# Kernel optimization log

Measured on AMD Instinct MI355X. Metric: run time of the kernel, lower is better.

Reference implementation:

```python
import jax, jax.numpy as jnp
import numpy as np

N_NODES = 100_000
N_EDGES = 6_400_000
CH = 5


def setup_inputs() -> dict:
    key = jax.random.key(0)
    ks = jax.random.split(key, 16)
    inp = {
        "x": jax.random.normal(ks[0], (N_NODES, 2), dtype=jnp.float32),
        "edge_index": jax.random.randint(ks[1], (2, N_EDGES), 0, N_NODES, dtype=jnp.int64 if jax.config.jax_enable_x64 else jnp.int32).astype(jnp.int32),
        "edge_attr": jax.random.uniform(ks[2], (N_EDGES, 1), dtype=jnp.float32),
        "lin1_w": jax.random.normal(ks[3], (2, CH), dtype=jnp.float32) * 0.5,
        "lin1_b": jax.random.normal(ks[4], (CH,), dtype=jnp.float32) * 0.1,
        "conv1_wf": jax.random.normal(ks[5], (2 * CH + 1, CH), dtype=jnp.float32) * 0.3,
        "conv1_bf": jax.random.normal(ks[6], (CH,), dtype=jnp.float32) * 0.1,
        "conv1_ws": jax.random.normal(ks[7], (2 * CH + 1, CH), dtype=jnp.float32) * 0.3,
        "conv1_bs": jax.random.normal(ks[8], (CH,), dtype=jnp.float32) * 0.1,
        "conv2_wf": jax.random.normal(ks[9], (2 * CH + 1, CH), dtype=jnp.float32) * 0.3,
        "conv2_bf": jax.random.normal(ks[10], (CH,), dtype=jnp.float32) * 0.1,
        "conv2_ws": jax.random.normal(ks[11], (2 * CH + 1, CH), dtype=jnp.float32) * 0.3,
        "conv2_bs": jax.random.normal(ks[12], (CH,), dtype=jnp.float32) * 0.1,
        "lin2_w": jax.random.normal(ks[13], (CH, 2), dtype=jnp.float32) * 0.5,
        "lin2_b": jax.random.normal(ks[14], (2,), dtype=jnp.float32) * 0.1,
    }
    return inp


def cgconv(x, edge_index, edge_attr, wf, bf, ws, bs):
    # PyG CGConv: x_i' = x_i + sum_{j->i} sigmoid(z W_f + b_f) * softplus(z W_s + b_s)
    # z = [x_i, x_j, e_ij]; edge_index[0]=source j, edge_index[1]=target i
    src, dst = edge_index[0], edge_index[1]
    z = jnp.concatenate([x[dst], x[src], edge_attr], axis=-1)  # [E, 2C+dim]
    msg = jax.nn.sigmoid(z @ wf + bf) * jax.nn.softplus(z @ ws + bs)  # [E, C]
    agg = jax.ops.segment_sum(msg, dst, num_segments=x.shape[0])  # [N, C]
    return x + agg


def reference(x, edge_index, edge_attr,
              lin1_w, lin1_b,
              conv1_wf, conv1_bf, conv1_ws, conv1_bs,
              conv2_wf, conv2_bf, conv2_ws, conv2_bs,
              lin2_w, lin2_b):
    h = x @ lin1_w + lin1_b  # [N, C]
    h = cgconv(h, edge_index, edge_attr, conv1_wf, conv1_bf, conv1_ws, conv1_bs)
    h = cgconv(h, edge_index, edge_attr, conv2_wf, conv2_bf, conv2_ws, conv2_bs)
    return h @ lin2_w + lin2_b  # [N, 2]
```

## Files before the change

### kernel.cpp

```cpp
#include <hip/hip_runtime.h>
#include <hip/hip_fp16.h>

constexpr int NN = 100000;
constexpr int NE = 6400000;
constexpr int BSH = 7;
constexpr int BN = 1 << BSH;
constexpr int NBUCK = (NN + BN - 1) / BN;
constexpr int BCAP = 9216;
constexpr int STILE = 8192;
constexpr int NSB = (NE + STILE - 1) / STILE;
constexpr int NP = 1024;

#define LOG2E 1.44269504f
#define LN2   0.69314718f


__device__ __forceinline__ void prep_core(const float hv[5],
                                          const float* __restrict__ wf,
                                          const float* __restrict__ bf,
                                          const float* __restrict__ ws,
                                          const float* __restrict__ bs,
                                          int n, float* __restrict__ TD,
                                          unsigned short* __restrict__ TSh) {
    float tg[5], ts[5], sg[5], ss[5];
#pragma unroll
    for (int c = 0; c < 5; ++c) {
        float a = bf[c], d = bs[c], u = 0.f, v = 0.f;
#pragma unroll
        for (int k = 0; k < 5; ++k) {
            a += hv[k] * wf[k * 5 + c];
            d += hv[k] * ws[k * 5 + c];
            u += hv[k] * wf[(5 + k) * 5 + c];
            v += hv[k] * ws[(5 + k) * 5 + c];
        }
        tg[c] = -a * LOG2E; ts[c] = -d * LOG2E;
        sg[c] = -u * LOG2E; ss[c] = -v * LOG2E;
    }
    float4* Dp = (float4*)(TD + (size_t)n * 12);
    Dp[0] = make_float4(tg[0], tg[1], tg[2], tg[3]);
    Dp[1] = make_float4(tg[4], ts[0], ts[1], ts[2]);
    Dp[2] = make_float4(ts[3], ts[4], 0.f, 0.f);

    unsigned p[5];
#pragma unroll
    for (int c = 0; c < 5; ++c) {
        unsigned lo = (unsigned)__half_as_ushort(__float2half_rn(sg[c]));
        unsigned hi = (unsigned)__half_as_ushort(__float2half_rn(ss[c]));
        p[c] = lo | (hi << 16);
    }
    uint4 w0 = make_uint4(p[0], p[1], p[2], p[3]);
    uint4 w1 = make_uint4(p[4], 0u, 0u, 0u);
    *(uint4*)(TSh + (size_t)n * 16) = w0;
    *(uint4*)(TSh + (size_t)n * 16 + 8) = w1;
}

__global__ __launch_bounds__(256) void k_prep1(const float* __restrict__ x,
                                               const float* __restrict__ l1w,
                                               const float* __restrict__ l1b,
                                               const float* __restrict__ wf,
                                               const float* __restrict__ bf,
                                               const float* __restrict__ ws,
                                               const float* __restrict__ bs,
                                               float* __restrict__ TD,
                                               unsigned short* __restrict__ TSh,
                                               float* __restrict__ h) {
    int n = blockIdx.x * 256 + threadIdx.x;
    if (n >= NN) return;
    float x0 = x[2 * n], x1 = x[2 * n + 1];
    float hv[5];
#pragma unroll
    for (int c = 0; c < 5; ++c) {
        hv[c] = l1b[c] + x0 * l1w[c] + x1 * l1w[5 + c];
        h[(size_t)n * 5 + c] = hv[c];
    }
    prep_core(hv, wf, bf, ws, bs, n, TD, TSh);
}

__global__ __launch_bounds__(256) void k_initcurs(int* __restrict__ gcurs) {
    int i = blockIdx.x * 256 + threadIdx.x;
    if (i < NBUCK) gcurs[i] = i * BCAP;
}

__global__ __launch_bounds__(512) void k_scatter4(const int* __restrict__ ei,
                                                  const float* __restrict__ ea,
                                                  int* __restrict__ gcurs,
                                                  unsigned int* __restrict__ rec) {
    __shared__ unsigned int lrec[STILE];
    __shared__ unsigned int spk[STILE];
    __shared__ int C[NBUCK];
    __shared__ int loc[NBUCK];
    __shared__ int gbase[NBUCK];
    __shared__ int A[NP];
    __shared__ int wsum[16];
    const int tid = threadIdx.x, blk = blockIdx.x;
    const int base = blk * STILE;
    const int m = min(STILE, NE - base);

    for (int i = tid; i < NBUCK; i += 512) C[i] = 0;
    __syncthreads();

    const int m4 = m >> 2;
    const int4* s4 = (const int4*)(ei + base);
    const int4* d4 = (const int4*)(ei + NE + base);
    const float4* a4 = (const float4*)(ea + base);
    for (int q = tid; q < m4; q += 512) {
        int4 s = s4[q];
        int4 d = d4[q];
        float4 a = a4[q];
        int k = q * 4;
        lrec[k + 0] = (unsigned)s.x | ((unsigned)(d.x & (BN - 1)) << 17) |
                      (__float2uint_rn(a.x * 255.f) << 24);
        lrec[k + 1] = (unsigned)s.y | ((unsigned)(d.y & (BN - 1)) << 17) |
                      (__float2uint_rn(a.y * 255.f) << 24);
        lrec[k + 2] = (unsigned)s.z | ((unsigned)(d.z & (BN - 1)) << 17) |
                      (__float2uint_rn(a.z * 255.f) << 24);
        lrec[k + 3] = (unsigned)s.w | ((unsigned)(d.w & (BN - 1)) << 17) |
                      (__float2uint_rn(a.w * 255.f) << 24);
        atomicAdd(&C[(unsigned)d.x >> BSH], 1);
        atomicAdd(&C[(unsigned)d.y >> BSH], 1);
        atomicAdd(&C[(unsigned)d.z >> BSH], 1);
        atomicAdd(&C[(unsigned)d.w >> BSH], 1);
    }
    __syncthreads();

    for (int b = tid; b < NBUCK; b += 512)
        gbase[b] = C[b] ? atomicAdd(&gcurs[b], C[b]) : 0;

    const int lane = tid & 63;
    const int wv = tid >> 6;
    int orig[2], incl[2];
#pragma unroll
    for (int half = 0; half < 2; ++half) {
        int c = wv + half * 8;
        int i = c * 64 + lane;
        int v = (i < NBUCK) ? C[i] : 0;
        orig[half] = v;
#pragma unroll
        for (int off = 1; off < 64; off <<= 1) {
            int t = __shfl_up(v, off, 64);
            if (lane >= off) v += t;
        }
        incl[half] = v;
        if (lane == 63) wsum[c] = v;
    }
    __syncthreads();
    if (tid < 16) {
        int v = wsum[tid];
#pragma unroll
        for (int off = 1; off < 16; off <<= 1) {
            int t = __shfl_up(v, off, 16);
            if (tid >= off) v += t;
        }
        wsum[tid] = v;
    }
    __syncthreads();
#pragma unroll
    for (int half = 0; half < 2; ++half) {
        int c = wv + half * 8;
        int i = c * 64 + lane;
        int coff = (c > 0) ? wsum[c - 1] : 0;
        int excl = incl[half] - orig[half] + coff;
        A[i] = excl;
        if (i < NBUCK) loc[i] = excl;
    }
    __syncthreads();

    for (int k = tid; k < m; k += 512) {
        int bkt = (unsigned)ei[NE + base + k] >> BSH;
        int p = atomicAdd(&loc[bkt], 1);
        spk[p] = (unsigned)k | ((unsigned)bkt << 16);
    }
    __syncthreads();

    for (int p = tid; p < m; p += 512) {
        unsigned pk = spk[p];
        int k = pk & 0xFFFF;
        int bkt = pk >> 16;
        rec[gbase[bkt] + (p - A[bkt])] = lrec[k];
    }
}

__global__ __launch_bounds__(512) void k_sortbkt(const int* __restrict__ gcurs,
                                                 unsigned int* __restrict__ rec,
                                                 int2* __restrict__ nrange) {
    __shared__ unsigned int lrec[BCAP];
    __shared__ int cnt[BN];
    __shared__ int curs[BN];
    const int b = blockIdx.x, tid = threadIdx.x;
    const int e0 = b * BCAP;
    const int m = gcurs[b] - e0;
    const int node0 = b << BSH;
    const int nloc = min(BN, NN - node0);

    for (int i = tid; i < m; i += 512) lrec[i] = rec[e0 + i];
    if (tid < BN) cnt[tid] = 0;
    __syncthreads();
    for (int i = tid; i < m; i += 512)
        atomicAdd(&cnt[(lrec[i] >> 17) & (BN - 1)], 1);
    __syncthreads();

    if (tid < 64) {
        int v0 = cnt[tid];
        int i0 = v0;
#pragma unroll
        for (int off = 1; off < 64; off <<= 1) {
            int t = __shfl_up(i0, off, 64);
            if (tid >= off) i0 += t;
        }
        int tot0 = __shfl(i0, 63, 64);
        int v1 = cnt[64 + tid];
        int i1 = v1;
#pragma unroll
        for (int off = 1; off < 64; off <<= 1) {
            int t = __shfl_up(i1, off, 64);
            if (tid >= off) i1 += t;
        }
        i1 += tot0;
        int e0x = i0 - v0;
        int e1x = i1 - v1;
        curs[tid] = e0x;
        curs[64 + tid] = e1x;
        if (tid < nloc)
            nrange[node0 + tid] = make_int2(e0 + e0x, e0 + e0x + v0);
        if (64 + tid < nloc)
            nrange[node0 + 64 + tid] = make_int2(e0 + e1x, e0 + e1x + v1);
    }
    __syncthreads();
    for (int i = tid; i < m; i += 512) {
        unsigned int r = lrec[i];
        int dl = (r >> 17) & (BN - 1);
        int pos = atomicAdd(&curs[dl], 1);
        rec[e0 + pos] = r;
    }
}

__device__ __forceinline__ void conv_core(
        const unsigned int* __restrict__ rec, const int2 rg,
        const float4* __restrict__ Dp, const unsigned short* __restrict__ TSh,
        const __half2 we2[5], float acc[5]) {
    const int lane = threadIdx.x & 15;
    float4 d0 = Dp[0], d1 = Dp[1], d2 = Dp[2];
    __half2 dd2[5];
    dd2[0] = __floats2half2_rn(d0.x, d1.y);
    dd2[1] = __floats2half2_rn(d0.y, d1.z);
    dd2[2] = __floats2half2_rn(d0.z, d1.w);
    dd2[3] = __floats2half2_rn(d0.w, d2.x);
    dd2[4] = __floats2half2_rn(d1.x, d2.y);
    const __half2 one2 = __float2half2_rn(1.f);
    const __half hz = __float2half(0.f);

#pragma unroll
    for (int c = 0; c < 5; ++c) acc[c] = 0.f;
    const int eEnd = rg.y;
    for (int e = rg.x + lane; e < eEnd; e += 64) {
        unsigned r[4];
        bool vld[4];
        float4 q0[4];
        unsigned q1[4];
        __half2 a2[4];
#pragma unroll
        for (int j = 0; j < 4; ++j) {
            int ej = e + j * 16;
            vld[j] = ej < eEnd;
            r[j] = rec[vld[j] ? ej : e];
        }
#pragma unroll
        for (int j = 0; j < 4; ++j) {
            const unsigned src = r[j] & 0x1FFFFu;
            const unsigned short* row = TSh + (size_t)src * 16;
            q0[j] = *(const float4*)row;
            q1[j] = *(const unsigned*)(row + 8);
            a2[j] = __float2half2_rn((float)(r[j] >> 24) * (1.f / 255.f));
        }
#pragma unroll
        for (int j = 0; j < 4; ++j) {
            if (!vld[j]) continue;
            union { float4 f; __half2 h2[4]; } u; u.f = q0[j];
            __half2 s2[5] = {u.h2[0], u.h2[1], u.h2[2], u.h2[3],
                             *(__half2*)&q1[j]};
#pragma unroll
            for (int c = 0; c < 5; ++c) {
                __half2 z2 = __hadd2(__hfma2(a2[j], we2[c], dd2[c]), s2[c]);
                __half zx = __low2half(z2);
                __half zy = __high2half(z2);
                __half nab = __hmin(zy, __hneg(zy));
                __half2 e2 = h2exp2(__halves2half2(zx, nab));
                __half2 o2 = __hadd2(e2, one2);
                float sig = __half2float(hrcp(__low2half(o2)));
                float lg  = __half2float(hlog2(__high2half(o2)));
                float mx  = __half2float(__hmin(zy, hz));
                acc[c] = fmaf(sig, lg - mx, acc[c]);
            }
        }
    }
#pragma unroll
    for (int off = 8; off >= 1; off >>= 1)
#pragma unroll
        for (int c = 0; c < 5; ++c)
            acc[c] += __shfl_xor(acc[c], off, 16);
}

__global__ __launch_bounds__(256) void k_conv_prep(
        const unsigned int* __restrict__ rec, const int2* __restrict__ nrange,
        const float* __restrict__ TD, const unsigned short* __restrict__ TSh,
        const float* __restrict__ wf, const float* __restrict__ ws,
        const float* __restrict__ wf2, const float* __restrict__ bf2,
        const float* __restrict__ ws2, const float* __restrict__ bs2,
        float* __restrict__ h,
        float* __restrict__ TD2, unsigned short* __restrict__ TSh2) {
    const int tid = threadIdx.x;
    const int lane = tid & 15;
    const int n = blockIdx.x * 16 + (tid >> 4);

    __half2 we2[5];
#pragma unroll
    for (int c = 0; c < 5; ++c)
        we2[c] = __floats2half2_rn(-wf[50 + c] * LOG2E, -ws[50 + c] * LOG2E);

    float acc[5];
    conv_core(rec, nrange[n], (const float4*)(TD + (size_t)n * 12), TSh,
              we2, acc);

    float hv[5];
#pragma unroll
    for (int c = 0; c < 5; ++c)
        hv[c] = h[(size_t)n * 5 + c] + LN2 * acc[c];
    if (lane == 0) {
#pragma unroll
        for (int c = 0; c < 5; ++c) h[(size_t)n * 5 + c] = hv[c];
    }
    if (lane < 5) {
        const int c = lane;
        float a = bf2[c], d = bs2[c], u = 0.f, v = 0.f;
#pragma unroll
        for (int k = 0; k < 5; ++k) {
            a += hv[k] * wf2[k * 5 + c];
            d += hv[k] * ws2[k * 5 + c];
            u += hv[k] * wf2[(5 + k) * 5 + c];
            v += hv[k] * ws2[(5 + k) * 5 + c];
        }
        TD2[(size_t)n * 12 + c]     = -a * LOG2E;
        TD2[(size_t)n * 12 + 5 + c] = -d * LOG2E;
        unsigned lo = (unsigned)__half_as_ushort(__float2half_rn(-u * LOG2E));
        unsigned hi = (unsigned)__half_as_ushort(__float2half_rn(-v * LOG2E));
        ((unsigned*)(TSh2 + (size_t)n * 16))[c] = lo | (hi << 16);
    }
}

__global__ __launch_bounds__(256) void k_conv_out(
        const unsigned int* __restrict__ rec, const int2* __restrict__ nrange,
        const float* __restrict__ TD, const unsigned short* __restrict__ TSh,
        const float* __restrict__ wf, const float* __restrict__ ws,
        const float* __restrict__ h,
        const float* __restrict__ l2w, const float* __restrict__ l2b,
        float* __restrict__ out) {
    const int tid = threadIdx.x;
    const int lane = tid & 15;
    const int n = blockIdx.x * 16 + (tid >> 4);

    __half2 we2[5];
#pragma unroll
    for (int c = 0; c < 5; ++c)
        we2[c] = __floats2half2_rn(-wf[50 + c] * LOG2E, -ws[50 + c] * LOG2E);

    float acc[5];
    conv_core(rec, nrange[n], (const float4*)(TD + (size_t)n * 12), TSh,
              we2, acc);

    if (lane == 0) {
        float o0 = l2b[0], o1 = l2b[1];
#pragma unroll
        for (int c = 0; c < 5; ++c) {
            float hv = h[(size_t)n * 5 + c] + LN2 * acc[c];
            o0 += hv * l2w[2 * c];
            o1 += hv * l2w[2 * c + 1];
        }
        out[2 * n] = o0;
        out[2 * n + 1] = o1;
    }
}

__global__ __launch_bounds__(256) void k_prep_fb(const float* __restrict__ h,
                                                 const float* __restrict__ wf,
                                                 const float* __restrict__ bf,
                                                 const float* __restrict__ ws,
                                                 const float* __restrict__ bs,
                                                 float* __restrict__ T,
                                                 float* __restrict__ S,
                                                 float* __restrict__ hout) {
    int n = blockIdx.x * 256 + threadIdx.x;
    if (n >= NN) return;
    float hv[5];
#pragma unroll
    for (int k = 0; k < 5; ++k) hv[k] = h[5 * n + k];
    float tf[5], ts[5], sf[5], ss[5];
#pragma unroll
    for (int c = 0; c < 5; ++c) {
        float a = bf[c], d = bs[c], u = 0.f, v = 0.f;
#pragma unroll
        for (int k = 0; k < 5; ++k) {
            a += hv[k] * wf[k * 5 + c];
            d += hv[k] * ws[k * 5 + c];
            u += hv[k] * wf[(5 + k) * 5 + c];
            v += hv[k] * ws[(5 + k) * 5 + c];
        }
        tf[c] = a; ts[c] = d; sf[c] = u; ss[c] = v;
    }
    float4* Tp = (float4*)(T + (size_t)n * 16);
    Tp[0] = make_float4(tf[0], tf[1], tf[2], tf[3]);
    Tp[1] = make_float4(tf[4], ts[0], ts[1], ts[2]);
    Tp[2] = make_float4(ts[3], ts[4], 0.f, 0.f);
    float4* Sp = (float4*)(S + (size_t)n * 16);
    Sp[0] = make_float4(sf[0], sf[1], sf[2], sf[3]);
    Sp[1] = make_float4(sf[4], ss[0], ss[1], ss[2]);
    Sp[2] = make_float4(ss[3], ss[4], 0.f, 0.f);
#pragma unroll
    for (int c = 0; c < 5; ++c) hout[5 * n + c] = hv[c];
}

__global__ __launch_bounds__(256) void k_conv_atomic(const int* __restrict__ ei,
                                                     const float* __restrict__ ea,
                                                     const float* __restrict__ T,
                                                     const float* __restrict__ S,
                                                     const float* __restrict__ wf,
                                                     const float* __restrict__ ws,
                                                     float* __restrict__ hout) {
    int e = blockIdx.x * 256 + threadIdx.x;
    if (e >= NE) return;
    int src = ei[e];
    int dst = ei[NE + e];
    float a = ea[e];
    const float4* Tp = (const float4*)(T + (size_t)dst * 16);
    const float4* Sp = (const float4*)(S + (size_t)src * 16);
    float4 t0 = Tp[0], t1 = Tp[1], t2 = Tp[2];
    float4 s0 = Sp[0], s1 = Sp[1], s2 = Sp[2];
    float za[5] = {t0.x + s0.x, t0.y + s0.y, t0.z + s0.z, t0.w + s0.w, t1.x + s1.x};
    float zs[5] = {t1.y + s1.y, t1.z + s1.z, t1.w + s1.w, t2.x + s2.x, t2.y + s2.y};
    float* outp = hout + (size_t)dst * 5;
#pragma unroll
    for (int c = 0; c < 5; ++c) {
        float f = za[c] + a * wf[50 + c];
        float s = zs[c] + a * ws[50 + c];
        float sig = 1.f / (1.f + __expf(-f));
        float sp = __logf(1.f + __expf(-fabsf(s))) + fmaxf(s, 0.f);
        unsafeAtomicAdd(outp + c, sig * sp);
    }
}

__global__ __launch_bounds__(256) void k_lin1_fb(const float* __restrict__ x,
                                                 const float* __restrict__ w,
                                                 const float* __restrict__ b,
                                                 float* __restrict__ h) {
    int n = blockIdx.x * 256 + threadIdx.x;
    if (n >= NN) return;
    float x0 = x[2 * n], x1 = x[2 * n + 1];
#pragma unroll
    for (int c = 0; c < 5; ++c)
        h[5 * n + c] = b[c] + x0 * w[c] + x1 * w[5 + c];
}

__global__ __launch_bounds__(256) void k_lin2_fb(const float* __restrict__ h,
                                                 const float* __restrict__ w,
                                                 const float* __restrict__ b,
                                                 float* __restrict__ out) {
    int n = blockIdx.x * 256 + threadIdx.x;
    if (n >= NN) return;
    float o0 = b[0], o1 = b[1];
#pragma unroll
    for (int c = 0; c < 5; ++c) {
        float hv = h[(size_t)n * 5 + c];
        o0 += hv * w[2 * c];
        o1 += hv * w[2 * c + 1];
    }
    out[2 * n] = o0;
    out[2 * n + 1] = o1;
}

extern "C" void kernel_launch(void* const* d_in, const int* in_sizes, int n_in,
                              void* d_out, int out_size, void* d_ws, size_t ws_size,
                              hipStream_t stream) {
    const float* x    = (const float*)d_in[0];
    const int*   ei   = (const int*)d_in[1];
    const float* ea   = (const float*)d_in[2];
    const float* l1w  = (const float*)d_in[3];
    const float* l1b  = (const float*)d_in[4];
    const float* c1wf = (const float*)d_in[5];
    const float* c1bf = (const float*)d_in[6];
    const float* c1ws = (const float*)d_in[7];
    const float* c1bs = (const float*)d_in[8];
    const float* c2wf = (const float*)d_in[9];
    const float* c2bf = (const float*)d_in[10];
    const float* c2ws = (const float*)d_in[11];
    const float* c2bs = (const float*)d_in[12];
    const float* l2w  = (const float*)d_in[13];
    const float* l2b  = (const float*)d_in[14];
    float* out = (float*)d_out;
    char* ws = (char*)d_ws;

    size_t o_rec    = 0;
    size_t o_nrange = o_rec + (size_t)NBUCK * BCAP * 4;
    size_t o_gcurs  = o_nrange + (size_t)NN * 8;
    size_t o_TD1    = (o_gcurs + (size_t)NBUCK * 4 + 15) & ~(size_t)15;
    size_t o_TS1    = o_TD1 + (size_t)NN * 12 * 4;
    size_t o_TD2    = o_TS1 + (size_t)NN * 16 * 2;
    size_t o_TS2    = o_TD2 + (size_t)NN * 12 * 4;
    size_t o_h      = o_TS2 + (size_t)NN * 16 * 2;
    size_t need     = o_h + (size_t)NN * 5 * 4;

    int nb_n = (NN + 255) / 256;

    if (ws_size >= need) {
        unsigned int* rec    = (unsigned int*)(ws + o_rec);
        int2* nrange         = (int2*)(ws + o_nrange);
        int* gcurs           = (int*)(ws + o_gcurs);
        float* TD1           = (float*)(ws + o_TD1);
        unsigned short* TS1  = (unsigned short*)(ws + o_TS1);
        float* TD2           = (float*)(ws + o_TD2);
        unsigned short* TS2  = (unsigned short*)(ws + o_TS2);
        float* h             = (float*)(ws + o_h);

        k_initcurs<<<(NBUCK + 255) / 256, 256, 0, stream>>>(gcurs);
        k_scatter4<<<NSB,   512, 0, stream>>>(ei, ea, gcurs, rec);
        k_sortbkt <<<NBUCK, 512, 0, stream>>>(gcurs, rec, nrange);

        k_prep1<<<nb_n, 256, 0, stream>>>(x, l1w, l1b,
                                          c1wf, c1bf, c1ws, c1bs, TD1, TS1, h);
        k_conv_prep<<<NN / 16, 256, 0, stream>>>(rec, nrange, TD1, TS1,
                                                 c1wf, c1ws,
                                                 c2wf, c2bf, c2ws, c2bs,
                                                 h, TD2, TS2);
        k_conv_out<<<NN / 16, 256, 0, stream>>>(rec, nrange, TD2, TS2,
                                                c2wf, c2ws, h, l2w, l2b, out);
    } else {
        float* h0 = (float*)(ws);
        float* h1 = (float*)(ws + 2000000);
        float* h2 = h0;
        float* T  = (float*)(ws + 4000000);
        float* S  = (float*)(ws + 10400000);
        int nb_e = (NE + 255) / 256;

        k_lin1_fb<<<nb_n, 256, 0, stream>>>(x, l1w, l1b, h0);
        k_prep_fb<<<nb_n, 256, 0, stream>>>(h0, c1wf, c1bf, c1ws, c1bs, T, S, h1);
        k_conv_atomic<<<nb_e, 256, 0, stream>>>(ei, ea, T, S, c1wf, c1ws, h1);
        k_prep_fb<<<nb_n, 256, 0, stream>>>(h1, c2wf, c2bf, c2ws, c2bs, T, S, h2);
        k_conv_atomic<<<nb_e, 256, 0, stream>>>(ei, ea, T, S, c2wf, c2ws, h2);
        k_lin2_fb<<<nb_n, 256, 0, stream>>>(h2, l2w, l2b, out);
    }
}
```

Baseline: 187.9 us.

## Drop per-node sort; aggregate each bucket's edges with shared-memory atomics

Removes the k_sortbkt pass that sorted each destination bucket by node and built per-node ranges. The conv kernels now run one 512-thread block per 128-node bucket, stream its unsorted edges, and accumulate messages into a shared-memory array with atomic adds, keeping destination terms in shared memory. This saves a full read/write pass over the edge records and the nrange array. The cost is heavy contention on shared-memory float atomics (about 64 edges per node, 5 channels), plus nondeterministic summation order and fewer, larger blocks (782).

```diff
diff --git a/kernel.cpp b/kernel.cpp
--- a/kernel.cpp
+++ b/kernel.cpp
@@ -180,198 +180,112 @@
     }
 }
 
-__global__ __launch_bounds__(512) void k_sortbkt(const int* __restrict__ gcurs,
-                                                 unsigned int* __restrict__ rec,
-                                                 int2* __restrict__ nrange) {
-    __shared__ unsigned int lrec[BCAP];
-    __shared__ int cnt[BN];
-    __shared__ int curs[BN];
-    const int b = blockIdx.x, tid = threadIdx.x;
-    const int e0 = b * BCAP;
-    const int m = gcurs[b] - e0;
-    const int node0 = b << BSH;
-    const int nloc = min(BN, NN - node0);
-
-    for (int i = tid; i < m; i += 512) lrec[i] = rec[e0 + i];
-    if (tid < BN) cnt[tid] = 0;
-    __syncthreads();
-    for (int i = tid; i < m; i += 512)
-        atomicAdd(&cnt[(lrec[i] >> 17) & (BN - 1)], 1);
-    __syncthreads();
-
-    if (tid < 64) {
-        int v0 = cnt[tid];
-        int i0 = v0;
-#pragma unroll
-        for (int off = 1; off < 64; off <<= 1) {
-            int t = __shfl_up(i0, off, 64);
-            if (tid >= off) i0 += t;
-        }
-        int tot0 = __shfl(i0, 63, 64);
-        int v1 = cnt[64 + tid];
-        int i1 = v1;
-#pragma unroll
-        for (int off = 1; off < 64; off <<= 1) {
-            int t = __shfl_up(i1, off, 64);
-            if (tid >= off) i1 += t;
-        }
-        i1 += tot0;
-        int e0x = i0 - v0;
-        int e1x = i1 - v1;
-        curs[tid] = e0x;
-        curs[64 + tid] = e1x;
-        if (tid < nloc)
-            nrange[node0 + tid] = make_int2(e0 + e0x, e0 + e0x + v0);
-        if (64 + tid < nloc)
-            nrange[node0 + 64 + tid] = make_int2(e0 + e1x, e0 + e1x + v1);
-    }
-    __syncthreads();
-    for (int i = tid; i < m; i += 512) {
-        unsigned int r = lrec[i];
-        int dl = (r >> 17) & (BN - 1);
-        int pos = atomicAdd(&curs[dl], 1);
-        rec[e0 + pos] = r;
-    }
-}
-
-__device__ __forceinline__ void conv_core(
-        const unsigned int* __restrict__ rec, const int2 rg,
-        const float4* __restrict__ Dp, const unsigned short* __restrict__ TSh,
-        const __half2 we2[5], float acc[5]) {
-    const int lane = threadIdx.x & 15;
-    float4 d0 = Dp[0], d1 = Dp[1], d2 = Dp[2];
-    __half2 dd2[5];
-    dd2[0] = __floats2half2_rn(d0.x, d1.y);
-    dd2[1] = __floats2half2_rn(d0.y, d1.z);
-    dd2[2] = __floats2half2_rn(d0.z, d1.w);
-    dd2[3] = __floats2half2_rn(d0.w, d2.x);
-    dd2[4] = __floats2half2_rn(d1.x, d2.y);
+__device__ __forceinline__ void bucket_conv_core(
+        const unsigned int* __restrict__ rec, int e0, int m,
+        const unsigned short* __restrict__ TSh,
+        const float* __restrict__ TD, int node0, int nloc,
+        const float* __restrict__ wf, const float* __restrict__ ws,
+        float* accf , __half2* sdd2 ) {
+    const int tid = threadIdx.x;
+    __half2 we2[5];
+#pragma unroll
+    for (int c = 0; c < 5; ++c)
+        we2[c] = __floats2half2_rn(-wf[50 + c] * LOG2E, -ws[50 + c] * LOG2E);
+
+    if (tid < nloc) {
+        const float4* Dp = (const float4*)(TD + (size_t)(node0 + tid) * 12);
+        float4 d0 = Dp[0], d1 = Dp[1], d2 = Dp[2];
+        sdd2[tid * 5 + 0] = __floats2half2_rn(d0.x, d1.y);
+        sdd2[tid * 5 + 1] = __floats2half2_rn(d0.y, d1.z);
+        sdd2[tid * 5 + 2] = __floats2half2_rn(d0.z, d1.w);
+        sdd2[tid * 5 + 3] = __floats2half2_rn(d0.w, d2.x);
+        sdd2[tid * 5 + 4] = __floats2half2_rn(d1.x, d2.y);
+    }
+    for (int i = tid; i < BN * 5; i += 512) accf[i] = 0.f;
+    __syncthreads();
+
     const __half2 one2 = __float2half2_rn(1.f);
     const __half hz = __float2half(0.f);
-
-#pragma unroll
-    for (int c = 0; c < 5; ++c) acc[c] = 0.f;
-    const int eEnd = rg.y;
-    for (int e = rg.x + lane; e < eEnd; e += 64) {
-        unsigned r[4];
-        bool vld[4];
-        float4 q0[4];
-        unsigned q1[4];
-        __half2 a2[4];
-#pragma unroll
-        for (int j = 0; j < 4; ++j) {
-            int ej = e + j * 16;
-            vld[j] = ej < eEnd;
-            r[j] = rec[vld[j] ? ej : e];
-        }
-#pragma unroll
-        for (int j = 0; j < 4; ++j) {
-            const unsigned src = r[j] & 0x1FFFFu;
-            const unsigned short* row = TSh + (size_t)src * 16;
-            q0[j] = *(const float4*)row;
-            q1[j] = *(const unsigned*)(row + 8);
-            a2[j] = __float2half2_rn((float)(r[j] >> 24) * (1.f / 255.f));
-        }
-#pragma unroll
-        for (int j = 0; j < 4; ++j) {
-            if (!vld[j]) continue;
-            union { float4 f; __half2 h2[4]; } u; u.f = q0[j];
-            __half2 s2[5] = {u.h2[0], u.h2[1], u.h2[2], u.h2[3],
-                             *(__half2*)&q1[j]};
-#pragma unroll
-            for (int c = 0; c < 5; ++c) {
-                __half2 z2 = __hadd2(__hfma2(a2[j], we2[c], dd2[c]), s2[c]);
-                __half zx = __low2half(z2);
-                __half zy = __high2half(z2);
-                __half nab = __hmin(zy, __hneg(zy));
-                __half2 e2 = h2exp2(__halves2half2(zx, nab));
-                __half2 o2 = __hadd2(e2, one2);
-                float sig = __half2float(hrcp(__low2half(o2)));
-                float lg  = __half2float(hlog2(__high2half(o2)));
-                float mx  = __half2float(__hmin(zy, hz));
-                acc[c] = fmaf(sig, lg - mx, acc[c]);
-            }
-        }
-    }
-#pragma unroll
-    for (int off = 8; off >= 1; off >>= 1)
-#pragma unroll
-        for (int c = 0; c < 5; ++c)
-            acc[c] += __shfl_xor(acc[c], off, 16);
-}
-
-__global__ __launch_bounds__(256) void k_conv_prep(
-        const unsigned int* __restrict__ rec, const int2* __restrict__ nrange,
+    for (int i = tid; i < m; i += 512) {
+        const unsigned r = rec[e0 + i];
+        const unsigned src = r & 0x1FFFFu;
+        const int dl = (r >> 17) & (BN - 1);
+        const unsigned short* row = TSh + (size_t)src * 16;
+        float4 q0 = *(const float4*)row;
+        unsigned q1 = *(const unsigned*)(row + 8);
+        __half2 a2 = __float2half2_rn((float)(r >> 24) * (1.f / 255.f));
+        union { float4 f; __half2 h2[4]; } u; u.f = q0;
+        __half2 s2[5] = {u.h2[0], u.h2[1], u.h2[2], u.h2[3], *(__half2*)&q1};
+#pragma unroll
+        for (int c = 0; c < 5; ++c) {
+            __half2 z2 = __hadd2(__hfma2(a2, we2[c], sdd2[dl * 5 + c]), s2[c]);
+            __half zx = __low2half(z2);
+            __half zy = __high2half(z2);
+            __half nab = __hmin(zy, __hneg(zy));
+            __half2 e2 = h2exp2(__halves2half2(zx, nab));
+            __half2 o2 = __hadd2(e2, one2);
+            float sig = __half2float(hrcp(__low2half(o2)));
+            float lg  = __half2float(hlog2(__high2half(o2)));
+            float mx  = __half2float(__hmin(zy, hz));
+            unsafeAtomicAdd(&accf[dl * 5 + c], sig * (lg - mx));
+        }
+    }
+    __syncthreads();
+}
+
+__global__ __launch_bounds__(512) void k_conv_prep(
+        const unsigned int* __restrict__ rec, const int* __restrict__ gcurs,
         const float* __restrict__ TD, const unsigned short* __restrict__ TSh,
         const float* __restrict__ wf, const float* __restrict__ ws,
         const float* __restrict__ wf2, const float* __restrict__ bf2,
         const float* __restrict__ ws2, const float* __restrict__ bs2,
         float* __restrict__ h,
         float* __restrict__ TD2, unsigned short* __restrict__ TSh2) {
-    const int tid = threadIdx.x;
-    const int lane = tid & 15;
-    const int n = blockIdx.x * 16 + (tid >> 4);
-
-    __half2 we2[5];
-#pragma unroll
-    for (int c = 0; c < 5; ++c)
-        we2[c] = __floats2half2_rn(-wf[50 + c] * LOG2E, -ws[50 + c] * LOG2E);
-
-    float acc[5];
-    conv_core(rec, nrange[n], (const float4*)(TD + (size_t)n * 12), TSh,
-              we2, acc);
-
-    float hv[5];
-#pragma unroll
-    for (int c = 0; c < 5; ++c)
-        hv[c] = h[(size_t)n * 5 + c] + LN2 * acc[c];
-    if (lane == 0) {
-#pragma unroll
-        for (int c = 0; c < 5; ++c) h[(size_t)n * 5 + c] = hv[c];
-    }
-    if (lane < 5) {
-        const int c = lane;
-        float a = bf2[c], d = bs2[c], u = 0.f, v = 0.f;
-#pragma unroll
-        for (int k = 0; k < 5; ++k) {
-            a += hv[k] * wf2[k * 5 + c];
-            d += hv[k] * ws2[k * 5 + c];
-            u += hv[k] * wf2[(5 + k) * 5 + c];
-            v += hv[k] * ws2[(5 + k) * 5 + c];
-        }
-        TD2[(size_t)n * 12 + c]     = -a * LOG2E;
-        TD2[(size_t)n * 12 + 5 + c] = -d * LOG2E;
-        unsigned lo = (unsigned)__half_as_ushort(__float2half_rn(-u * LOG2E));
-        unsigned hi = (unsigned)__half_as_ushort(__float2half_rn(-v * LOG2E));
-        ((unsigned*)(TSh2 + (size_t)n * 16))[c] = lo | (hi << 16);
-    }
-}
-
-__global__ __launch_bounds__(256) void k_conv_out(
-        const unsigned int* __restrict__ rec, const int2* __restrict__ nrange,
+    __shared__ float accf[BN * 5];
+    __shared__ __half2 sdd2[BN * 5];
+    const int b = blockIdx.x, tid = threadIdx.x;
+    const int e0 = b * BCAP;
+    const int m = gcurs[b] - e0;
+    const int node0 = b << BSH;
+    const int nloc = min(BN, NN - node0);
+
+    bucket_conv_core(rec, e0, m, TSh, TD, node0, nloc, wf, ws, accf, sdd2);
+
+    if (tid < nloc) {
+        const int n = node0 + tid;
+        float hv[5];
+#pragma unroll
+        for (int c = 0; c < 5; ++c) {
+            hv[c] = h[(size_t)n * 5 + c] + LN2 * accf[tid * 5 + c];
+            h[(size_t)n * 5 + c] = hv[c];
+        }
+        prep_core(hv, wf2, bf2, ws2, bs2, n, TD2, TSh2);
+    }
+}
+
+__global__ __launch_bounds__(512) void k_conv_out(
+        const unsigned int* __restrict__ rec, const int* __restrict__ gcurs,
         const float* __restrict__ TD, const unsigned short* __restrict__ TSh,
         const float* __restrict__ wf, const float* __restrict__ ws,
         const float* __restrict__ h,
         const float* __restrict__ l2w, const float* __restrict__ l2b,
         float* __restrict__ out) {
-    const int tid = threadIdx.x;
-    const int lane = tid & 15;
-    const int n = blockIdx.x * 16 + (tid >> 4);
-
-    __half2 we2[5];
-#pragma unroll
-    for (int c = 0; c < 5; ++c)
-        we2[c] = __floats2half2_rn(-wf[50 + c] * LOG2E, -ws[50 + c] * LOG2E);
-
-    float acc[5];
-    conv_core(rec, nrange[n], (const float4*)(TD + (size_t)n * 12), TSh,
-              we2, acc);
-
-    if (lane == 0) {
+    __shared__ float accf[BN * 5];
+    __shared__ __half2 sdd2[BN * 5];
+    const int b = blockIdx.x, tid = threadIdx.x;
+    const int e0 = b * BCAP;
+    const int m = gcurs[b] - e0;
+    const int node0 = b << BSH;
+    const int nloc = min(BN, NN - node0);
+
+    bucket_conv_core(rec, e0, m, TSh, TD, node0, nloc, wf, ws, accf, sdd2);
+
+    if (tid < nloc) {
+        const int n = node0 + tid;
         float o0 = l2b[0], o1 = l2b[1];
 #pragma unroll
         for (int c = 0; c < 5; ++c) {
-            float hv = h[(size_t)n * 5 + c] + LN2 * acc[c];
+            float hv = h[(size_t)n * 5 + c] + LN2 * accf[tid * 5 + c];
             o0 += hv * l2w[2 * c];
             o1 += hv * l2w[2 * c + 1];
         }
@@ -498,8 +412,7 @@
     char* ws = (char*)d_ws;
 
     size_t o_rec    = 0;
-    size_t o_nrange = o_rec + (size_t)NBUCK * BCAP * 4;
-    size_t o_gcurs  = o_nrange + (size_t)NN * 8;
+    size_t o_gcurs  = o_rec + (size_t)NBUCK * BCAP * 4;
     size_t o_TD1    = (o_gcurs + (size_t)NBUCK * 4 + 15) & ~(size_t)15;
     size_t o_TS1    = o_TD1 + (size_t)NN * 12 * 4;
     size_t o_TD2    = o_TS1 + (size_t)NN * 16 * 2;
@@ -511,7 +424,6 @@
 
     if (ws_size >= need) {
         unsigned int* rec    = (unsigned int*)(ws + o_rec);
-        int2* nrange         = (int2*)(ws + o_nrange);
         int* gcurs           = (int*)(ws + o_gcurs);
         float* TD1           = (float*)(ws + o_TD1);
         unsigned short* TS1  = (unsigned short*)(ws + o_TS1);
@@ -520,17 +432,16 @@
         float* h             = (float*)(ws + o_h);
 
         k_initcurs<<<(NBUCK + 255) / 256, 256, 0, stream>>>(gcurs);
-        k_scatter4<<<NSB,   512, 0, stream>>>(ei, ea, gcurs, rec);
-        k_sortbkt <<<NBUCK, 512, 0, stream>>>(gcurs, rec, nrange);
+        k_scatter4<<<NSB, 512, 0, stream>>>(ei, ea, gcurs, rec);
 
         k_prep1<<<nb_n, 256, 0, stream>>>(x, l1w, l1b,
                                           c1wf, c1bf, c1ws, c1bs, TD1, TS1, h);
-        k_conv_prep<<<NN / 16, 256, 0, stream>>>(rec, nrange, TD1, TS1,
-                                                 c1wf, c1ws,
-                                                 c2wf, c2bf, c2ws, c2bs,
-                                                 h, TD2, TS2);
-        k_conv_out<<<NN / 16, 256, 0, stream>>>(rec, nrange, TD2, TS2,
-                                                c2wf, c2ws, h, l2w, l2b, out);
+        k_conv_prep<<<NBUCK, 512, 0, stream>>>(rec, gcurs, TD1, TS1,
+                                               c1wf, c1ws,
+                                               c2wf, c2bf, c2ws, c2bs,
+                                               h, TD2, TS2);
+        k_conv_out<<<NBUCK, 512, 0, stream>>>(rec, gcurs, TD2, TS2,
+                                              c2wf, c2ws, h, l2w, l2b, out);
     } else {
         float* h0 = (float*)(ws);
         float* h1 = (float*)(ws + 2000000);
```

Result: slower. 494.4 us (+163.1%).
